# Performance work log

Hardware: AMD Instinct MI355X
Metric: run time of the kernel (lower is better)

Reference implementation:

```python
import jax, jax.numpy as jnp
import numpy as np

B, I, O, ORDER = 16384, 256, 256, 8
LO, HI = -1.0, 1.0


def setup_inputs() -> dict:
    key = jax.random.key(0)
    k1, k2, k3 = jax.random.split(key, 3)
    x = jax.random.normal(k1, (B, I), dtype=jnp.float32)
    weights = jax.random.normal(k2, (O, I), dtype=jnp.float32)
    # BernsteinBasisFunction init: randn(order+1) * 0.1, one per (o, i) pair
    coeffs = jax.random.normal(k3, (O, I, ORDER + 1), dtype=jnp.float32) * 0.1
    return {"x": x, "weights": weights, "coeffs": coeffs}


def reference(x, weights, coeffs):
    # x: [B, I]; weights: [O, I]; coeffs: [O, I, K+1]
    K = coeffs.shape[-1] - 1
    zoom = (HI - LO) / 2.0
    pan = (HI + LO) / 2.0
    xt = jnp.tanh(x) * zoom + pan          # squash into [LO, HI]
    x_a = xt - LO                          # [B, I]
    x_b = HI - xt                          # [B, I]
    e = jnp.arange(K + 1)
    # ber[b, i, k] = x_a^k * x_b^(K-k)  (unnormalized Bernstein basis)
    ber = (x_a[..., None] ** e) * (x_b[..., None] ** (K - e))  # [B, I, K+1]
    # transformed[b, o, i] = sum_k coeffs[o,i,k] * ber[b,i,k]; out = einsum('boi,oi->bo')
    # Fused: fold weights into coeffs to avoid the [B, O, I] intermediate.
    wc = coeffs * weights[..., None]       # [O, I, K+1]
    return jnp.einsum('bik,oik->bo', ber, wc)
```

## Files before the change

kernel.cpp:

```cpp
#include <hip/hip_runtime.h>
#include <hip/hip_bf16.h>


#define BDIM 16384
#define IDIM 256
#define ODIM 256
#define NK 9
#define NCHUNK 4
#define NSTEP 36
#define STEP_ELEMS (ODIM * 64)
#define CGW 4

typedef short short8 __attribute__((ext_vector_type(8)));
typedef float floatx4 __attribute__((ext_vector_type(4)));

__global__ __launch_bounds__(256) void prep_wc2(const float* __restrict__ weights,
                                                const float* __restrict__ coeffs,
                                                ushort* __restrict__ wc) {
    int idx  = blockIdx.x * 256 + threadIdx.x;
    int step = idx >> 11;
    int c    = idx & 2047;
    int big    = c >> 6;
    int lane_w = c & 63;
    int o    = (big >> 1) * 16 + (lane_w & 15);
    int s    = big & 1;
    int quad = lane_w >> 4;
    int ic = step / 9;
    int k  = step - ic * 9;
    int i0 = ic * 64 + s * 32 + quad * 8;

    const float* cp = coeffs + (size_t)(o * IDIM + i0) * NK + k;
    float4 w0 = *(const float4*)(weights + o * IDIM + i0);
    float4 w1 = *(const float4*)(weights + o * IDIM + i0 + 4);
    float wv[8] = {w0.x, w0.y, w0.z, w0.w, w1.x, w1.y, w1.z, w1.w};

    union { ushort us[8]; int4 v; __hip_bfloat162 h2[4]; } pk;
#pragma unroll
    for (int j = 0; j < 8; j += 2) {
        float a = cp[(size_t)j * NK] * wv[j];
        float b = cp[(size_t)(j + 1) * NK] * wv[j + 1];
        pk.h2[j >> 1] = __float22bfloat162_rn(make_float2(a, b));
    }
    *(int4*)(wc + (size_t)step * STEP_ELEMS + (size_t)c * 8) = pk.v;
}

__global__ __launch_bounds__(512, 2) void bern_gemm(const float* __restrict__ x,
                                                    const ushort* __restrict__ wc,
                                                    float* __restrict__ out) {
    __shared__ ushort Blds[2][16384];

    const int tid  = threadIdx.x;
    const int wave = tid >> 6;
    const int lane = tid & 63;
    const int cg   = blockIdx.x & 3;
    const int rb   = (blockIdx.x >> 2) * 256 + wave * 32;
    const int lrow = lane & 15;
    const int jseg = (lane >> 4) * 8;

    float p[2][2][8];
    float r[2][2][8];
    floatx4 acc[2][4];
    floatx4 zero = {0.0f, 0.0f, 0.0f, 0.0f};
#pragma unroll
    for (int m = 0; m < 2; ++m)
#pragma unroll
        for (int n = 0; n < 4; ++n)
            acc[m][n] = zero;

#define LOAD_X(ic_)                                                             \
    {                                                                           \
        _Pragma("unroll") for (int m = 0; m < 2; ++m)                           \
        _Pragma("unroll") for (int s = 0; s < 2; ++s) {                         \
            const float* xp = x + (size_t)(rb + m * 16 + lrow) * IDIM           \
                              + (ic_) * 64 + s * 32 + jseg;                     \
            float4 v0 = *(const float4*)(xp);                                   \
            float4 v1 = *(const float4*)(xp + 4);                               \
            p[m][s][0] = v0.x; p[m][s][1] = v0.y;                               \
            p[m][s][2] = v0.z; p[m][s][3] = v0.w;                               \
            p[m][s][4] = v1.x; p[m][s][5] = v1.y;                               \
            p[m][s][6] = v1.z; p[m][s][7] = v1.w;                               \
        }                                                                       \
    }

#define SETUP_BASIS()                                                           \
    {                                                                           \
        _Pragma("unroll") for (int m = 0; m < 2; ++m)                           \
        _Pragma("unroll") for (int s = 0; s < 2; ++s)                           \
        _Pragma("unroll") for (int e = 0; e < 8; ++e) {                         \
            float t  = __builtin_amdgcn_exp2f(p[m][s][e] * 2.8853900817779268f);\
            float q  = 2.0f * __builtin_amdgcn_rcpf(t + 1.0f);                  \
            float q2 = q * q;                                                   \
            float q4 = q2 * q2;                                                 \
            p[m][s][e] = q4 * q4;                                               \
            r[m][s][e] = t;                                                     \
        }                                                                       \
    }

#define STAGE(g_, b_)                                                           \
    {                                                                           \
        _Pragma("unroll") for (int q = 0; q < 4; ++q) {                         \
            int st  = (g_) * 4 + q;                                             \
            const ushort* sp = wc + (size_t)st * STEP_ELEMS + cg * 4096         \
                               + wave * 512 + lane * 8;                         \
            ushort* dp = &Blds[b_][(q * 8 + wave) * 512 + lane * 8];            \
            __builtin_amdgcn_global_load_lds(                                   \
                (const __attribute__((address_space(1))) void*)sp,              \
                (__attribute__((address_space(3))) void*)dp, 16, 0, 0);         \
        }                                                                       \
    }

    LOAD_X(0);
    SETUP_BASIS();
    STAGE(0, 0);

#pragma unroll
    for (int g = 0; g < 9; ++g) {
        __syncthreads();
        if (g < 8) STAGE(g + 1, (g + 1) & 1);

#pragma unroll
        for (int k4 = 0; k4 < 4; ++k4) {
            const int step = g * 4 + k4;
            if (step == 9 || step == 18 || step == 27) {
                LOAD_X(step / 9);
                SETUP_BASIS();
            }
            const int kin = step % 9;

#pragma unroll
            for (int s = 0; s < 2; ++s) {
                short8 bfr[4];
#pragma unroll
                for (int n = 0; n < 4; ++n)
                    bfr[n] = *(const short8*)&Blds[g & 1]
                        [k4 * 4096 + (n * 2 + s) * 512 + lane * 8];

#pragma unroll
                for (int m = 0; m < 2; ++m) {
                    union { ushort us[8]; short8 v; __hip_bfloat162 h2[4]; } pk;
#pragma unroll
                    for (int e = 0; e < 8; e += 2) {
                        pk.h2[e >> 1] = __float22bfloat162_rn(
                            make_float2(p[m][s][e], p[m][s][e + 1]));
                    }
#pragma unroll
                    for (int n = 0; n < 4; ++n)
                        acc[m][n] = __builtin_amdgcn_mfma_f32_16x16x32_bf16(
                            pk.v, bfr[n], acc[m][n], 0, 0, 0);
                    if (kin < NK - 1)
#pragma unroll
                        for (int e = 0; e < 8; ++e) p[m][s][e] *= r[m][s][e];
                }
            }
        }
    }

#pragma unroll
    for (int m = 0; m < 2; ++m) {
#pragma unroll
        for (int n = 0; n < 4; ++n) {
            int col   = cg * 64 + n * 16 + (lane & 15);
            int rbase = rb + m * 16 + (lane >> 4) * 4;
#pragma unroll
            for (int reg = 0; reg < 4; ++reg) {
                out[(size_t)(rbase + reg) * ODIM + col] = acc[m][n][reg];
            }
        }
    }
#undef LOAD_X
#undef SETUP_BASIS
#undef STAGE
}

extern "C" void kernel_launch(void* const* d_in, const int* in_sizes, int n_in,
                              void* d_out, int out_size, void* d_ws, size_t ws_size,
                              hipStream_t stream) {
    const float* x       = (const float*)d_in[0];
    const float* weights = (const float*)d_in[1];
    const float* coeffs  = (const float*)d_in[2];
    float* out = (float*)d_out;
    ushort* wc = (ushort*)d_ws;

    prep_wc2<<<288, 256, 0, stream>>>(weights, coeffs, wc);
    bern_gemm<<<256, 512, 0, stream>>>(x, wc, out);
}
```

Before: 98.47 us.

## Halve GEMM block size and prefetch next x chunk during last basis step

Reduces bern_gemm blocks to 4 waves covering 128 rows each and doubles the grid, with each wave staging two B-tile segments into LDS. The x values for the next input chunk are now loaded into the ratio registers during the final basis step of the current chunk, and the tanh-based basis setup runs after that step's MFMAs, hiding global-load latency. The smaller block doubles the amount of weight-tile staging per output row while giving the scheduler more, smaller blocks.

```diff
diff --git a/kernel.cpp b/kernel.cpp
--- a/kernel.cpp
+++ b/kernel.cpp
@@ -44,7 +44,7 @@
     *(int4*)(wc + (size_t)step * STEP_ELEMS + (size_t)c * 8) = pk.v;
 }
 
-__global__ __launch_bounds__(512, 2) void bern_gemm(const float* __restrict__ x,
+__global__ __launch_bounds__(256, 2) void bern_gemm(const float* __restrict__ x,
                                                     const ushort* __restrict__ wc,
                                                     float* __restrict__ out) {
     __shared__ ushort Blds[2][16384];
@@ -53,7 +53,7 @@
     const int wave = tid >> 6;
     const int lane = tid & 63;
     const int cg   = blockIdx.x & 3;
-    const int rb   = (blockIdx.x >> 2) * 256 + wave * 32;
+    const int rb   = (blockIdx.x >> 2) * 128 + wave * 32;
     const int lrow = lane & 15;
     const int jseg = (lane >> 4) * 8;
 
@@ -67,7 +67,7 @@
         for (int n = 0; n < 4; ++n)
             acc[m][n] = zero;
 
-#define LOAD_X(ic_)                                                             \
+#define LOAD_XR(ic_)                                                            \
     {                                                                           \
         _Pragma("unroll") for (int m = 0; m < 2; ++m)                           \
         _Pragma("unroll") for (int s = 0; s < 2; ++s) {                         \
@@ -75,19 +75,19 @@
                               + (ic_) * 64 + s * 32 + jseg;                     \
             float4 v0 = *(const float4*)(xp);                                   \
             float4 v1 = *(const float4*)(xp + 4);                               \
-            p[m][s][0] = v0.x; p[m][s][1] = v0.y;                               \
-            p[m][s][2] = v0.z; p[m][s][3] = v0.w;                               \
-            p[m][s][4] = v1.x; p[m][s][5] = v1.y;                               \
-            p[m][s][6] = v1.z; p[m][s][7] = v1.w;                               \
+            r[m][s][0] = v0.x; r[m][s][1] = v0.y;                               \
+            r[m][s][2] = v0.z; r[m][s][3] = v0.w;                               \
+            r[m][s][4] = v1.x; r[m][s][5] = v1.y;                               \
+            r[m][s][6] = v1.z; r[m][s][7] = v1.w;                               \
         }                                                                       \
     }
 
-#define SETUP_BASIS()                                                           \
+#define SETUP_FROM_R()                                                          \
     {                                                                           \
         _Pragma("unroll") for (int m = 0; m < 2; ++m)                           \
         _Pragma("unroll") for (int s = 0; s < 2; ++s)                           \
         _Pragma("unroll") for (int e = 0; e < 8; ++e) {                         \
-            float t  = __builtin_amdgcn_exp2f(p[m][s][e] * 2.8853900817779268f);\
+            float t  = __builtin_amdgcn_exp2f(r[m][s][e] * 2.8853900817779268f);\
             float q  = 2.0f * __builtin_amdgcn_rcpf(t + 1.0f);                  \
             float q2 = q * q;                                                   \
             float q4 = q2 * q2;                                                 \
@@ -98,19 +98,20 @@
 
 #define STAGE(g_, b_)                                                           \
     {                                                                           \
-        _Pragma("unroll") for (int q = 0; q < 4; ++q) {                         \
+        _Pragma("unroll") for (int q = 0; q < 4; ++q)                           \
+        _Pragma("unroll") for (int h = 0; h < 2; ++h) {                         \
             int st  = (g_) * 4 + q;                                             \
-            const ushort* sp = wc + (size_t)st * STEP_ELEMS + cg * 4096         \
-                               + wave * 512 + lane * 8;                         \
-            ushort* dp = &Blds[b_][(q * 8 + wave) * 512 + lane * 8];            \
+            int off = wave * 1024 + h * 512 + lane * 8;                         \
+            const ushort* sp = wc + (size_t)st * STEP_ELEMS + cg * 4096 + off;  \
+            ushort* dp = &Blds[b_][q * 4096 + off];                             \
             __builtin_amdgcn_global_load_lds(                                   \
                 (const __attribute__((address_space(1))) void*)sp,              \
                 (__attribute__((address_space(3))) void*)dp, 16, 0, 0);         \
         }                                                                       \
     }
 
-    LOAD_X(0);
-    SETUP_BASIS();
+    LOAD_XR(0);
+    SETUP_FROM_R();
     STAGE(0, 0);
 
 #pragma unroll
@@ -121,9 +122,8 @@
 #pragma unroll
         for (int k4 = 0; k4 < 4; ++k4) {
             const int step = g * 4 + k4;
-            if (step == 9 || step == 18 || step == 27) {
-                LOAD_X(step / 9);
-                SETUP_BASIS();
+            if (step == 8 || step == 17 || step == 26) {
+                LOAD_XR(step / 9 + 1);
             }
             const int kin = step % 9;
 
@@ -152,6 +152,10 @@
                         for (int e = 0; e < 8; ++e) p[m][s][e] *= r[m][s][e];
                 }
             }
+
+            if (step == 8 || step == 17 || step == 26) {
+                SETUP_FROM_R();
+            }
         }
     }
 
@@ -167,8 +171,8 @@
             }
         }
     }
-#undef LOAD_X
-#undef SETUP_BASIS
+#undef LOAD_XR
+#undef SETUP_FROM_R
 #undef STAGE
 }
 
@@ -182,5 +186,5 @@
     ushort* wc = (ushort*)d_ws;
 
     prep_wc2<<<288, 256, 0, stream>>>(weights, coeffs, wc);
-    bern_gemm<<<256, 512, 0, stream>>>(x, wc, out);
+    bern_gemm<<<512, 256, 0, stream>>>(x, wc, out);
 }
```

Result: no change. 98.48 us (+0.0%).

## Triple-buffer LDS weight staging and prefetch x chunks ahead with explicit vmcnt waits

Applied to the files above, without the earlier changes.

Moves the shared-memory weight staging from double to triple buffering, issuing loads two groups ahead. Replaces __syncthreads with explicit s_waitcnt vmcnt counts plus a raw s_barrier. The x chunk for the next input block is now loaded into separate registers several groups early, and the basis is set up right after the previous chunk finishes, so global load latency is hidden behind MFMA work. The cost is 96KB of LDS per block (risking the 2-blocks-per-CU occupancy target), extra registers for the prefetched x, and fragile hand-counted vmcnt values.

```diff
diff --git a/kernel.cpp b/kernel.cpp
--- a/kernel.cpp
+++ b/kernel.cpp
@@ -6,10 +6,8 @@
 #define IDIM 256
 #define ODIM 256
 #define NK 9
-#define NCHUNK 4
 #define NSTEP 36
 #define STEP_ELEMS (ODIM * 64)
-#define CGW 4
 
 typedef short short8 __attribute__((ext_vector_type(8)));
 typedef float floatx4 __attribute__((ext_vector_type(4)));
@@ -47,7 +45,7 @@
 __global__ __launch_bounds__(512, 2) void bern_gemm(const float* __restrict__ x,
                                                     const ushort* __restrict__ wc,
                                                     float* __restrict__ out) {
-    __shared__ ushort Blds[2][16384];
+    __shared__ ushort Blds[3][16384];
 
     const int tid  = threadIdx.x;
     const int wave = tid >> 6;
@@ -59,6 +57,7 @@
 
     float p[2][2][8];
     float r[2][2][8];
+    float xq[2][2][8];
     floatx4 acc[2][4];
     floatx4 zero = {0.0f, 0.0f, 0.0f, 0.0f};
 #pragma unroll
@@ -67,7 +66,7 @@
         for (int n = 0; n < 4; ++n)
             acc[m][n] = zero;
 
-#define LOAD_X(ic_)                                                             \
+#define LOAD_XQ(ic_)                                                            \
     {                                                                           \
         _Pragma("unroll") for (int m = 0; m < 2; ++m)                           \
         _Pragma("unroll") for (int s = 0; s < 2; ++s) {                         \
@@ -75,19 +74,19 @@
                               + (ic_) * 64 + s * 32 + jseg;                     \
             float4 v0 = *(const float4*)(xp);                                   \
             float4 v1 = *(const float4*)(xp + 4);                               \
-            p[m][s][0] = v0.x; p[m][s][1] = v0.y;                               \
-            p[m][s][2] = v0.z; p[m][s][3] = v0.w;                               \
-            p[m][s][4] = v1.x; p[m][s][5] = v1.y;                               \
-            p[m][s][6] = v1.z; p[m][s][7] = v1.w;                               \
+            xq[m][s][0] = v0.x; xq[m][s][1] = v0.y;                             \
+            xq[m][s][2] = v0.z; xq[m][s][3] = v0.w;                             \
+            xq[m][s][4] = v1.x; xq[m][s][5] = v1.y;                             \
+            xq[m][s][6] = v1.z; xq[m][s][7] = v1.w;                             \
         }                                                                       \
     }
 
-#define SETUP_BASIS()                                                           \
+#define SETUP_FROM_XQ()                                                         \
     {                                                                           \
         _Pragma("unroll") for (int m = 0; m < 2; ++m)                           \
         _Pragma("unroll") for (int s = 0; s < 2; ++s)                           \
         _Pragma("unroll") for (int e = 0; e < 8; ++e) {                         \
-            float t  = __builtin_amdgcn_exp2f(p[m][s][e] * 2.8853900817779268f);\
+            float t  = __builtin_amdgcn_exp2f(xq[m][s][e] * 2.8853900817779268f);\
             float q  = 2.0f * __builtin_amdgcn_rcpf(t + 1.0f);                  \
             float q2 = q * q;                                                   \
             float q4 = q2 * q2;                                                 \
@@ -100,31 +99,39 @@
     {                                                                           \
         _Pragma("unroll") for (int q = 0; q < 4; ++q) {                         \
             int st  = (g_) * 4 + q;                                             \
-            const ushort* sp = wc + (size_t)st * STEP_ELEMS + cg * 4096         \
-                               + wave * 512 + lane * 8;                         \
-            ushort* dp = &Blds[b_][(q * 8 + wave) * 512 + lane * 8];            \
+            int off = wave * 512 + lane * 8;                                    \
+            const ushort* sp = wc + (size_t)st * STEP_ELEMS + cg * 4096 + off;  \
+            ushort* dp = &Blds[b_][q * 4096 + off];                             \
             __builtin_amdgcn_global_load_lds(                                   \
                 (const __attribute__((address_space(1))) void*)sp,              \
                 (__attribute__((address_space(3))) void*)dp, 16, 0, 0);         \
         }                                                                       \
     }
 
-    LOAD_X(0);
-    SETUP_BASIS();
+#define WAITV(n_) asm volatile("s_waitcnt vmcnt(" #n_ ")" ::: "memory")
+
+    LOAD_XQ(0);
+    SETUP_FROM_XQ();
     STAGE(0, 0);
+    STAGE(1, 1);
 
 #pragma unroll
     for (int g = 0; g < 9; ++g) {
-        __syncthreads();
-        if (g < 8) STAGE(g + 1, (g + 1) & 1);
+        if (g == 2 || g == 4 || g == 6) { WAITV(12); }
+        else if (g == 8)                { WAITV(0);  }
+        else                            { WAITV(4);  }
+        __builtin_amdgcn_s_barrier();
+        __builtin_amdgcn_sched_barrier(0);
 
+        if (g == 1) LOAD_XQ(1);
+        if (g == 3) LOAD_XQ(2);
+        if (g == 5) LOAD_XQ(3);
+        if (g < 7) STAGE(g + 2, (g + 2) % 3);
+
+        const int bg = g % 3;
 #pragma unroll
         for (int k4 = 0; k4 < 4; ++k4) {
             const int step = g * 4 + k4;
-            if (step == 9 || step == 18 || step == 27) {
-                LOAD_X(step / 9);
-                SETUP_BASIS();
-            }
             const int kin = step % 9;
 
 #pragma unroll
@@ -132,7 +139,7 @@
                 short8 bfr[4];
 #pragma unroll
                 for (int n = 0; n < 4; ++n)
-                    bfr[n] = *(const short8*)&Blds[g & 1]
+                    bfr[n] = *(const short8*)&Blds[bg]
                         [k4 * 4096 + (n * 2 + s) * 512 + lane * 8];
 
 #pragma unroll
@@ -152,6 +159,10 @@
                         for (int e = 0; e < 8; ++e) p[m][s][e] *= r[m][s][e];
                 }
             }
+
+            if (step == 8 || step == 17 || step == 26) {
+                SETUP_FROM_XQ();
+            }
         }
     }
 
@@ -167,9 +178,10 @@
             }
         }
     }
-#undef LOAD_X
-#undef SETUP_BASIS
+#undef LOAD_XQ
+#undef SETUP_FROM_XQ
 #undef STAGE
+#undef WAITV
 }
 
 extern "C" void kernel_launch(void* const* d_in, const int* in_sizes, int n_in,
```

Measured after the change: 97.99 us. Within noise of the previous version (-0.5%).
